# Optimization experiments

Measured on AMD Instinct MI355X. Metric: run time of the kernel, lower is better.

The kernel has to match this reference:

```python
import jax, jax.numpy as jnp
import numpy as np

# --- constants matching DILConfig ---
N_DIFF = 1000      # num_diffusion_steps
STEPS = 4          # inference_steps
S_MAX = 4          # max_scales
BUDGET = 0.2       # entropy_budget
G0 = 2.0           # guidance_strength
ENT_LO = 0.1       # stability_threshold_low
ENT_HI = 0.5       # stability_threshold_high
B, L, C, H = 16, 1024, 128, 512


def setup_inputs() -> dict:
    key = jax.random.key(0)
    ks = jax.random.split(key, 6)
    y_obs = jax.random.normal(ks[0], (B, L, C), dtype=jnp.float32)
    mask = (jax.random.uniform(ks[1], (B, L, C)) > 0.5).astype(jnp.float32)
    z_init = jax.random.normal(ks[2], (B, L, C), dtype=jnp.float32)
    W1 = jax.random.normal(ks[3], (C, H), dtype=jnp.float32) / np.sqrt(C)
    b1 = jnp.zeros((H,), dtype=jnp.float32)
    W2 = jax.random.normal(ks[4], (H, C), dtype=jnp.float32) / np.sqrt(H)
    b2 = jnp.zeros((C,), dtype=jnp.float32)
    tw = jax.random.normal(ks[5], (H,), dtype=jnp.float32)
    return {"y_obs": y_obs, "mask": mask, "z_init": z_init,
            "W1": W1, "b1": b1, "W2": W2, "b2": b2, "tw": tw}


def _dil_forward(y_obs, mask, z_init, W1, b1, W2, b2, tw):
    # diffusion schedule (linear betas)
    betas = jnp.linspace(1e-4, 0.02, N_DIFF, dtype=jnp.float32)
    ac = jnp.cumprod(1.0 - betas)
    alpha = jnp.sqrt(ac)                     # sqrt_alphas_cumprod
    sigma = jnp.sqrt(1.0 - ac)               # sqrt_one_minus_alphas_cumprod
    lam = jnp.log(alpha) - jnp.log(sigma)    # log-SNR/2

    step = N_DIFF // STEPS
    ks = [N_DIFF - 1 - i * step for i in range(STEPS)]

    def score(z, k):
        # epsilon predictor: channel MLP with scalar time feature
        t_feat = jnp.float32(k) / N_DIFF
        h = jax.nn.gelu(jnp.einsum('blc,ch->blh', z, W1) + b1 + t_feat * tw)
        return jnp.einsum('blh,hc->blc', h, W2) + b2

    z = z_init
    for k in ks:  # fixed small unrolled loop over inference steps
        kp = max(k - step, 0)
        eps = score(z, k)                                   # [B,L,C]
        h_lam = lam[kp] - lam[k]
        base_a = alpha[kp] / alpha[k]
        base_b = sigma[kp] * (jnp.exp(h_lam) - 1.0)

        # entropy map: batch-mean |eps| per pixel
        ent_pix = jnp.mean(jnp.abs(eps), axis=0)            # [L,C]

        # self-guidance on observed entries
        obs_err = (z - y_obs) * mask
        guidance = -obs_err / (jnp.var(obs_err) + 1e-8)     # [B,L,C]

        z_new = z
        # coarse -> fine so finer-scale selected nodes overwrite coarser ones
        for s in range(S_MAX - 1, -1, -1):
            w = 2 ** s
            pooled = ent_pix.reshape(L // w, w, C // w, w).mean(axis=(1, 3))
            Knodes = max(1, int(BUDGET * pooled.size))
            _, idx = jax.lax.top_k(pooled.ravel(), Knodes)
            selg = jnp.zeros((pooled.size,), jnp.float32).at[idx].set(1.0)
            selg = selg.reshape(pooled.shape)
            sel = jnp.repeat(jnp.repeat(selg, w, axis=0), w, axis=1)     # [L,C]
            ent_up = jnp.repeat(jnp.repeat(pooled, w, axis=0), w, axis=1)

            # adaptive solver order from entropy stability thresholds
            order = (1.0 + (ent_up > ENT_LO).astype(jnp.float32)
                         + (ent_up > ENT_HI).astype(jnp.float32))
            corr = (1.0 + (order - 1.0) * 0.5 * h_lam
                        + (order - 1.0) * (order - 2.0) / 6.0 * h_lam ** 2)
            gs = G0 * ent_up / (ent_up + 1.0)               # adaptive guidance

            cand = base_a * z - base_b * (corr * eps) + gs * guidance
            z_new = jnp.where(sel[None, :, :] > 0, cand, z_new)
        z = z_new
    return z


def reference(y_obs, mask, z_init, W1, b1, W2, b2, tw):
    return _dil_forward(y_obs, mask, z_init, W1, b1, W2, b2, tw)
```

## Files before the change

### kernel.cpp

```cpp
#include <hip/hip_runtime.h>
#include <math.h>
#include <stdint.h>

#define L_DIM 1024
#define C_DIM 128
#define H_DIM 512
#define B_DIM 16
#define LC (L_DIM * C_DIM)
#define BLC (B_DIM * LC)

typedef __attribute__((ext_vector_type(8))) short short8;
typedef __attribute__((ext_vector_type(4))) float floatx4;

__device__ __forceinline__ unsigned fordbits(unsigned u) {
    return (u & 0x80000000u) ? ~u : (u | 0x80000000u);
}

__device__ __forceinline__ void split3(float x, unsigned& uh, unsigned& um,
                                       unsigned& ul) {
    uh = __float_as_uint(x);
    const float r1 = x - __uint_as_float(uh & 0xffff0000u);
    um = __float_as_uint(r1);
    const float r2 = r1 - __uint_as_float(um & 0xffff0000u);
    ul = __float_as_uint(r2);
}

__device__ __forceinline__ float gelu_fast(float x) {
    const float g = 0.7978845608028654f * (x + 0.044715f * x * x * x);
    const float e = __expf(2.0f * g);
    const float t = 1.0f - 2.0f / (e + 1.0f);
    return 0.5f * x * (1.0f + t);
}

__global__ __launch_bounds__(256) void wsplit_kernel(
    const float* __restrict__ W1, const float* __restrict__ W2,
    unsigned short* __restrict__ W1h, unsigned short* __restrict__ W1m,
    unsigned short* __restrict__ W1l, unsigned short* __restrict__ W2h,
    unsigned short* __restrict__ W2m, unsigned short* __restrict__ W2l) {
    const int t = blockIdx.x * 256 + threadIdx.x;
    unsigned uh, um, ul;
    if (t < 65536) {
        const int j = t & 7, lane = (t >> 3) & 63, nt = (t >> 9) & 31,
                  kt = (t >> 14) & 3;
        const int k = kt * 32 + (lane >> 4) * 8 + j;
        const int n = nt * 16 + (lane & 15);
        split3(W1[k * 512 + n], uh, um, ul);
        W1h[t] = (unsigned short)(uh >> 16);
        W1m[t] = (unsigned short)(um >> 16);
        W1l[t] = (unsigned short)(ul >> 16);
    } else {
        const int t2 = t - 65536;
        const int j = t2 & 7, lane = (t2 >> 3) & 63, nt = (t2 >> 9) & 7,
                  kt = (t2 >> 12) & 15;
        const int k = kt * 32 + (lane >> 4) * 8 + j;
        const int n = nt * 16 + (lane & 15);
        split3(W2[k * 128 + n], uh, um, ul);
        W2h[t2] = (unsigned short)(uh >> 16);
        W2m[t2] = (unsigned short)(um >> 16);
        W2l[t2] = (unsigned short)(ul >> 16);
    }
}

#define MFMA6(AH, AM, AL, BH, BM, BL, ACC)                                    \
    ACC = __builtin_amdgcn_mfma_f32_16x16x32_bf16(AL, BH, ACC, 0, 0, 0);      \
    ACC = __builtin_amdgcn_mfma_f32_16x16x32_bf16(AM, BM, ACC, 0, 0, 0);      \
    ACC = __builtin_amdgcn_mfma_f32_16x16x32_bf16(AH, BL, ACC, 0, 0, 0);      \
    ACC = __builtin_amdgcn_mfma_f32_16x16x32_bf16(AM, BH, ACC, 0, 0, 0);      \
    ACC = __builtin_amdgcn_mfma_f32_16x16x32_bf16(AH, BM, ACC, 0, 0, 0);      \
    ACC = __builtin_amdgcn_mfma_f32_16x16x32_bf16(AH, BH, ACC, 0, 0, 0);

__device__ __forceinline__ int swz(int row, int col) {
    return row * 128 + ((((col >> 3) ^ (row & 15))) << 3) + (col & 7);
}

template <int UPD>
__global__ __launch_bounds__(512, 4) void mlp_kernel(
    float* __restrict__ z, const float* __restrict__ y,
    const float* __restrict__ mk,
    const unsigned short* __restrict__ W1h, const unsigned short* __restrict__ W1m,
    const unsigned short* __restrict__ W1l, const unsigned short* __restrict__ W2h,
    const unsigned short* __restrict__ W2m, const unsigned short* __restrict__ W2l,
    const float* __restrict__ b1, const float* __restrict__ tw,
    const float* __restrict__ b2, float t_feat,
    float* __restrict__ eps_buf, float* __restrict__ ent,
    const float* __restrict__ cA, const float* __restrict__ cB,
    const float* __restrict__ cG, float* __restrict__ accum) {
    __shared__ unsigned short zA[3][4096];
    __shared__ unsigned short hA[3][4096];
    __shared__ float red1[8], red2[8];
    const int tid = threadIdx.x;
    const int w = tid >> 6, lane = tid & 63;
    const int quad = lane >> 4, m16 = lane & 15;
    const int l0 = blockIdx.x * 2;

    float s1 = 0.f, s2 = 0.f;
#pragma unroll
    for (int e = 0; e < 2; ++e) {
        const int f = tid * 8 + e * 4;
        const int r_ = f >> 7, cb = f & 127;
        const int b = r_ & 15, il = r_ >> 4, l = l0 + il;
        const size_t g = ((size_t)b * 1024 + l) * 128 + cb;
        float4 zv = *(const float4*)(z + g);
        const float4 yv = *(const float4*)(y + g);
        const float4 mv = *(const float4*)(mk + g);
        if (UPD) {
            const float4 ev = *(const float4*)(eps_buf + g);
            const int pix = l * 128 + cb;
            const float4 a4 = *(const float4*)(cA + pix);
            const float4 b4 = *(const float4*)(cB + pix);
            const float4 g4 = *(const float4*)(cG + pix);
            zv.x = a4.x * zv.x - b4.x * ev.x - g4.x * ((zv.x - yv.x) * mv.x);
            zv.y = a4.y * zv.y - b4.y * ev.y - g4.y * ((zv.y - yv.y) * mv.y);
            zv.z = a4.z * zv.z - b4.z * ev.z - g4.z * ((zv.z - yv.z) * mv.z);
            zv.w = a4.w * zv.w - b4.w * ev.w - g4.w * ((zv.w - yv.w) * mv.w);
            *(float4*)(z + g) = zv;
        }
        float oe;
        oe = (zv.x - yv.x) * mv.x; s1 += oe; s2 += oe * oe;
        oe = (zv.y - yv.y) * mv.y; s1 += oe; s2 += oe * oe;
        oe = (zv.z - yv.z) * mv.z; s1 += oe; s2 += oe * oe;
        oe = (zv.w - yv.w) * mv.w; s1 += oe; s2 += oe * oe;

        const int base = swz(r_, cb);
        const float xs[4] = {zv.x, zv.y, zv.z, zv.w};
        ushort4 vh, vm, vl;
        unsigned uh, um, ul;
        split3(xs[0], uh, um, ul); vh.x = uh >> 16; vm.x = um >> 16; vl.x = ul >> 16;
        split3(xs[1], uh, um, ul); vh.y = uh >> 16; vm.y = um >> 16; vl.y = ul >> 16;
        split3(xs[2], uh, um, ul); vh.z = uh >> 16; vm.z = um >> 16; vl.z = ul >> 16;
        split3(xs[3], uh, um, ul); vh.w = uh >> 16; vm.w = um >> 16; vl.w = ul >> 16;
        *(ushort4*)(&zA[0][base]) = vh;
        *(ushort4*)(&zA[1][base]) = vm;
        *(ushort4*)(&zA[2][base]) = vl;
    }
#pragma unroll
    for (int off = 32; off; off >>= 1) {
        s1 += __shfl_down(s1, off);
        s2 += __shfl_down(s2, off);
    }
    if (lane == 0) { red1[w] = s1; red2[w] = s2; }
    __syncthreads();
    if (tid == 0) {
        float a1 = 0.f, a2 = 0.f;
#pragma unroll
        for (int i = 0; i < 8; ++i) { a1 += red1[i]; a2 += red2[i]; }
        atomicAdd(&accum[0], a1);
        atomicAdd(&accum[1], a2);
    }

    floatx4 acc1[8];
#pragma unroll
    for (int i = 0; i < 8; ++i) acc1[i] = (floatx4){0.f, 0.f, 0.f, 0.f};

#pragma unroll
    for (int kt = 0; kt < 4; ++kt) {
        short8 Ah[2], Am[2], Al[2];
#pragma unroll
        for (int il = 0; il < 2; ++il) {
            const int fb = swz(il * 16 + m16, kt * 32 + quad * 8);
            Ah[il] = *(const short8*)(&zA[0][fb]);
            Am[il] = *(const short8*)(&zA[1][fb]);
            Al[il] = *(const short8*)(&zA[2][fb]);
        }
#pragma unroll
        for (int q = 0; q < 4; ++q) {
            const size_t off = ((size_t)(kt * 32 + q * 8 + w) * 64 + lane) * 8;
            const short8 bh = *(const short8*)(W1h + off);
            const short8 bm = *(const short8*)(W1m + off);
            const short8 bl = *(const short8*)(W1l + off);
#pragma unroll
            for (int il = 0; il < 2; ++il) {
                floatx4 a = acc1[q * 2 + il];
                MFMA6(Ah[il], Am[il], Al[il], bh, bm, bl, a);
                acc1[q * 2 + il] = a;
            }
        }
    }

    floatx4 acc2[2];
    acc2[0] = (floatx4){0.f, 0.f, 0.f, 0.f};
    acc2[1] = (floatx4){0.f, 0.f, 0.f, 0.f};

    for (int q = 0; q < 4; ++q) {
        __syncthreads();
        {
            const int colg = q * 128 + w * 16 + m16;
            const float bb = b1[colg] + t_feat * tw[colg];
            const int kcol = w * 16 + m16;
#pragma unroll
            for (int il = 0; il < 2; ++il) {
#pragma unroll
                for (int r = 0; r < 4; ++r) {
                    const float x = gelu_fast(acc1[q * 2 + il][r] + bb);
                    unsigned uh, um, ul;
                    split3(x, uh, um, ul);
                    const int idx = swz(il * 16 + quad * 4 + r, kcol);
                    hA[0][idx] = (unsigned short)(uh >> 16);
                    hA[1][idx] = (unsigned short)(um >> 16);
                    hA[2][idx] = (unsigned short)(ul >> 16);
                }
            }
        }
        __syncthreads();

#pragma unroll
        for (int ktl = 0; ktl < 4; ++ktl) {
            short8 Ah2[2], Am2[2], Al2[2];
#pragma unroll
            for (int il = 0; il < 2; ++il) {
                const int fb = swz(il * 16 + m16, ktl * 32 + quad * 8);
                Ah2[il] = *(const short8*)(&hA[0][fb]);
                Am2[il] = *(const short8*)(&hA[1][fb]);
                Al2[il] = *(const short8*)(&hA[2][fb]);
            }
            const size_t off =
                ((size_t)((q * 4 + ktl) * 8 + w) * 64 + lane) * 8;
            const short8 bh = *(const short8*)(W2h + off);
            const short8 bm = *(const short8*)(W2m + off);
            const short8 bl = *(const short8*)(W2l + off);
#pragma unroll
            for (int il = 0; il < 2; ++il) {
                floatx4 a = acc2[il];
                MFMA6(Ah2[il], Am2[il], Al2[il], bh, bm, bl, a);
                acc2[il] = a;
            }
        }
    }

    {
        const int col = w * 16 + m16;
        const float bb2 = b2[col];
#pragma unroll
        for (int il = 0; il < 2; ++il) {
            float pa = 0.f;
#pragma unroll
            for (int r = 0; r < 4; ++r) {
                const float e = acc2[il][r] + bb2;
                const int b = quad * 4 + r;
                eps_buf[((size_t)b * 1024 + l0 + il) * 128 + col] = e;
                pa += fabsf(e);
            }
            pa += __shfl_xor(pa, 16);
            pa += __shfl_xor(pa, 32);
            if (quad == 0) ent[(l0 + il) * 128 + col] = pa * (1.0f / 16.0f);
        }
    }
}

__device__ __forceinline__ void grid_barrier(unsigned* c, unsigned* r) {
    __syncthreads();
    if (threadIdx.x == 0) {
        __threadfence();
        if (atomicAdd(c, 1u) + 1u == 85u) atomicExch(r, 1u);
        else
            while (atomicAdd(r, 0u) == 0u) __builtin_amdgcn_s_sleep(8);
    }
    __syncthreads();
}

__global__ __launch_bounds__(256, 1) void select_kernel(
    const float* __restrict__ ent, float* __restrict__ p1,
    float* __restrict__ p2, float* __restrict__ p3,
    unsigned* __restrict__ ghist, unsigned* __restrict__ ctr,
    unsigned* __restrict__ rel, unsigned* __restrict__ gprefix,
    float* __restrict__ cA, float* __restrict__ cB, float* __restrict__ cG,
    const float* __restrict__ accum_si, float base_a, float base_b,
    float h_lam, int si) {
    const int bid = blockIdx.x, t = threadIdx.x;
    const int gid = bid * 256 + t;
    const int slot0 = si * 6;

    for (int i = gid; i < 32768; i += 21760) {
        const int r = i >> 6, c = i & 63;
        float s = 0.f;
#pragma unroll
        for (int ii = 0; ii < 2; ++ii)
#pragma unroll
            for (int jj = 0; jj < 2; ++jj)
                s += ent[((r * 2 + ii) << 7) + c * 2 + jj];
        atomicExch((unsigned*)&p1[i], __float_as_uint(s * 0.25f));
    }
    for (int i = gid; i < 8192; i += 21760) {
        const int r = i >> 5, c = i & 31;
        float s = 0.f;
#pragma unroll
        for (int ii = 0; ii < 4; ++ii)
#pragma unroll
            for (int jj = 0; jj < 4; ++jj)
                s += ent[((r * 4 + ii) << 7) + c * 4 + jj];
        atomicExch((unsigned*)&p2[i], __float_as_uint(s * 0.0625f));
    }
    for (int i = gid; i < 2048; i += 21760) {
        const int r = i >> 4, c = i & 15;
        float s = 0.f;
#pragma unroll
        for (int ii = 0; ii < 8; ++ii)
#pragma unroll
            for (int jj = 0; jj < 8; ++jj)
                s += ent[((r * 8 + ii) << 7) + c * 8 + jj];
        atomicExch((unsigned*)&p3[i], __float_as_uint(s * (1.0f / 64.0f)));
    }
    grid_barrier(&ctr[slot0], &rel[slot0]);

    const float* data;
    int scale, base;
    unsigned K;
    if (bid < 64) { scale = 0; data = ent; base = bid * 2048; K = 26214u; }
    else if (bid < 80) { scale = 1; data = p1; base = (bid - 64) * 2048; K = 6553u; }
    else if (bid < 84) { scale = 2; data = p2; base = (bid - 80) * 2048; K = 1638u; }
    else { scale = 3; data = p3; base = 0; K = 409u; }

    __shared__ unsigned hist[4][256];
    __shared__ unsigned sh[256];
    __shared__ unsigned sh_dig, sh_krem;
    const int wv = t >> 6;
    unsigned prefix = 0u, krem = K;

    for (int p = 0; p < 4; ++p) {
        const int shift = 24 - 8 * p;
        const unsigned hmask = p ? (0xFFFFFFFFu << (shift + 8)) : 0u;
#pragma unroll
        for (int i = t; i < 1024; i += 256) ((unsigned*)hist)[i] = 0u;
        __syncthreads();
#pragma unroll
        for (int i = t; i < 2048; i += 256) {
            const unsigned raw = atomicAdd((unsigned*)&data[base + i], 0u);
            const unsigned u = fordbits(raw);
            if ((u & hmask) == (prefix & hmask))
                atomicAdd(&hist[wv][(u >> shift) & 255u], 1u);
        }
        __syncthreads();
        const unsigned c = hist[0][t] + hist[1][t] + hist[2][t] + hist[3][t];
        unsigned* gh = &ghist[((si * 4 + p) * 4 + scale) * 256];
        if (c) atomicAdd(&gh[t], c);
        grid_barrier(&ctr[slot0 + 1 + p], &rel[slot0 + 1 + p]);
        sh[t] = atomicAdd(&gh[t], 0u);
        __syncthreads();
#pragma unroll
        for (int off = 1; off < 256; off <<= 1) {
            const unsigned v = (t + off < 256) ? sh[t + off] : 0u;
            __syncthreads();
            sh[t] += v;
            __syncthreads();
        }
        const unsigned suf = sh[t];
        const unsigned sufn = (t < 255) ? sh[t + 1] : 0u;
        if (suf >= krem && sufn < krem) {
            sh_dig = (unsigned)t;
            sh_krem = krem - sufn;
        }
        __syncthreads();
        prefix |= (sh_dig << shift);
        krem = sh_krem;
        __syncthreads();
    }
    if (t == 0 && base == 0) atomicExch(&gprefix[scale], prefix);
    grid_barrier(&ctr[slot0 + 5], &rel[slot0 + 5]);

    const unsigned t0 = atomicAdd(&gprefix[0], 0u);
    const unsigned t1 = atomicAdd(&gprefix[1], 0u);
    const unsigned t2 = atomicAdd(&gprefix[2], 0u);
    const unsigned t3 = atomicAdd(&gprefix[3], 0u);
    const float mean = accum_si[0] * (1.0f / (float)BLC);
    const float var = accum_si[1] * (1.0f / (float)BLC) - mean * mean;
    const float vinv = 1.0f / (var + 1e-8f);

    for (int i = gid; i < LC; i += 21760) {
        const int l = i >> 7, c = i & 127;
        float ent_v = 0.f;
        bool sel = false;
        const float v0 = ent[i];
        if (fordbits(__float_as_uint(v0)) >= t0) { ent_v = v0; sel = true; }
        else {
            const float v1 = __uint_as_float(atomicAdd(
                (unsigned*)&p1[((l >> 1) << 6) + (c >> 1)], 0u));
            if (fordbits(__float_as_uint(v1)) >= t1) { ent_v = v1; sel = true; }
            else {
                const float v2 = __uint_as_float(atomicAdd(
                    (unsigned*)&p2[((l >> 2) << 5) + (c >> 2)], 0u));
                if (fordbits(__float_as_uint(v2)) >= t2) { ent_v = v2; sel = true; }
                else {
                    const float v3 = __uint_as_float(atomicAdd(
                        (unsigned*)&p3[((l >> 3) << 4) + (c >> 3)], 0u));
                    if (fordbits(__float_as_uint(v3)) >= t3) { ent_v = v3; sel = true; }
                }
            }
        }
        if (sel) {
            float corr;
            if (ent_v > 0.5f)
                corr = 1.0f + h_lam + h_lam * h_lam * (1.0f / 3.0f);
            else if (ent_v > 0.1f)
                corr = 1.0f + 0.5f * h_lam;
            else
                corr = 1.0f;
            cA[i] = base_a;
            cB[i] = base_b * corr;
            cG[i] = (2.0f * ent_v / (ent_v + 1.0f)) * vinv;
        } else {
            cA[i] = 1.0f;
            cB[i] = 0.f;
            cG[i] = 0.f;
        }
    }
}

__global__ __launch_bounds__(256) void update_kernel(
    float* __restrict__ z, const float* __restrict__ y,
    const float* __restrict__ mk, const float* __restrict__ eps,
    const float* __restrict__ cA, const float* __restrict__ cB,
    const float* __restrict__ cG) {
    const int idx = blockIdx.x * 256 + threadIdx.x;
    const int p = idx & (LC - 1);
    const float zi = z[idx];
    z[idx] = cA[p] * zi - cB[p] * eps[idx] - cG[p] * ((zi - y[idx]) * mk[idx]);
}

extern "C" void kernel_launch(void* const* d_in, const int* in_sizes, int n_in,
                              void* d_out, int out_size, void* d_ws,
                              size_t ws_size, hipStream_t stream) {
    const float* y_obs = (const float*)d_in[0];
    const float* mask = (const float*)d_in[1];
    const float* z_init = (const float*)d_in[2];
    const float* W1 = (const float*)d_in[3];
    const float* b1 = (const float*)d_in[4];
    const float* W2 = (const float*)d_in[5];
    const float* b2 = (const float*)d_in[6];
    const float* tw = (const float*)d_in[7];
    float* z = (float*)d_out;
    float* ws = (float*)d_ws;

    float* eps = ws;
    float* ent = ws + 2097152;
    float* p1 = ws + 2228224;
    float* p2 = ws + 2260992;
    float* p3 = ws + 2269184;
    float* cA = ws + 2271232;
    float* cB = ws + 2402304;
    float* cG = ws + 2533376;
    unsigned* ghist = (unsigned*)(ws + 2664448);
    unsigned* ctr = (unsigned*)(ws + 2680832);
    unsigned* rel = (unsigned*)(ws + 2680856);
    float* accum = ws + 2680880;
    unsigned* gprefix = (unsigned*)(ws + 2680888);
    unsigned short* W1h = (unsigned short*)(ws + 2680896);
    unsigned short* W1m = (unsigned short*)(ws + 2713664);
    unsigned short* W1l = (unsigned short*)(ws + 2746432);
    unsigned short* W2h = (unsigned short*)(ws + 2779200);
    unsigned short* W2m = (unsigned short*)(ws + 2811968);
    unsigned short* W2l = (unsigned short*)(ws + 2844736);

    float alpha_[1000], sigma_[1000], lam_[1000];
    {
        float ac = 1.0f;
        for (int i = 0; i < 1000; ++i) {
            const float beta = 1e-4f + (0.02f - 1e-4f) * ((float)i / 999.0f);
            ac = ac * (1.0f - beta);
            alpha_[i] = sqrtf(ac);
            sigma_[i] = sqrtf(1.0f - ac);
            lam_[i] = logf(alpha_[i]) - logf(sigma_[i]);
        }
    }
    float tf[4], hl[4], ba[4], bb[4];
    for (int si = 0; si < 4; ++si) {
        const int k = 999 - si * 250;
        const int kp = (k - 250 > 0) ? (k - 250) : 0;
        tf[si] = (float)k / 1000.0f;
        hl[si] = lam_[kp] - lam_[k];
        ba[si] = alpha_[kp] / alpha_[k];
        bb[si] = sigma_[kp] * (expf(hl[si]) - 1.0f);
    }

    hipMemcpyAsync(z, z_init, sizeof(float) * BLC, hipMemcpyDeviceToDevice,
                   stream);
    hipMemsetAsync(ghist, 0, (16384 + 24 + 24 + 8 + 4) * sizeof(unsigned),
                   stream);
    wsplit_kernel<<<512, 256, 0, stream>>>(W1, W2, W1h, W1m, W1l, W2h, W2m,
                                           W2l);

    for (int si = 0; si < 4; ++si) {
        if (si == 0) {
            mlp_kernel<0><<<512, 512, 0, stream>>>(
                z, y_obs, mask, W1h, W1m, W1l, W2h, W2m, W2l, b1, tw, b2,
                tf[0], eps, ent, cA, cB, cG, accum);
        } else {
            mlp_kernel<1><<<512, 512, 0, stream>>>(
                z, y_obs, mask, W1h, W1m, W1l, W2h, W2m, W2l, b1, tw, b2,
                tf[si], eps, ent, cA, cB, cG, accum + 2 * si);
        }
        select_kernel<<<85, 256, 0, stream>>>(
            ent, p1, p2, p3, ghist, ctr, rel, gprefix, cA, cB, cG,
            accum + 2 * si, ba[si], bb[si], hl[si], si);
    }
    update_kernel<<<8192, 256, 0, stream>>>(z, y_obs, mask, eps, cA, cB, cG);
}
```

Measured before the change: 407.1 us.

## Fuse pooling into radix-select blocks, cache data in LDS, simplify grid barrier

Each select block now computes its own slice of the pooled entropy maps directly into shared memory, so the first grid barrier is gone and histogram passes read LDS instead of doing atomic global reads. The grid barrier becomes a single monotonically increasing counter per step with cumulative targets and a shorter sleep, and the fence is dropped. The grid grows to 88 blocks so the coarsest scale is split across four blocks. Removing the threadfence risks weaker memory ordering for the global histogram and prefix values.

```diff
diff --git a/kernel.cpp b/kernel.cpp
--- a/kernel.cpp
+++ b/kernel.cpp
@@ -247,13 +247,11 @@
     }
 }
 
-__device__ __forceinline__ void grid_barrier(unsigned* c, unsigned* r) {
+__device__ __forceinline__ void gbar(unsigned* c, unsigned target) {
     __syncthreads();
     if (threadIdx.x == 0) {
-        __threadfence();
-        if (atomicAdd(c, 1u) + 1u == 85u) atomicExch(r, 1u);
-        else
-            while (atomicAdd(r, 0u) == 0u) __builtin_amdgcn_s_sleep(8);
+        atomicAdd(c, 1u);
+        while (atomicAdd(c, 0u) < target) __builtin_amdgcn_s_sleep(1);
     }
     __syncthreads();
 }
@@ -262,70 +260,85 @@
     const float* __restrict__ ent, float* __restrict__ p1,
     float* __restrict__ p2, float* __restrict__ p3,
     unsigned* __restrict__ ghist, unsigned* __restrict__ ctr,
-    unsigned* __restrict__ rel, unsigned* __restrict__ gprefix,
-    float* __restrict__ cA, float* __restrict__ cB, float* __restrict__ cG,
+    unsigned* __restrict__ gprefix, float* __restrict__ cA,
+    float* __restrict__ cB, float* __restrict__ cG,
     const float* __restrict__ accum_si, float base_a, float base_b,
     float h_lam, int si) {
-    const int bid = blockIdx.x, t = threadIdx.x;
-    const int gid = bid * 256 + t;
-    const int slot0 = si * 6;
-
-    for (int i = gid; i < 32768; i += 21760) {
-        const int r = i >> 6, c = i & 63;
-        float s = 0.f;
-#pragma unroll
-        for (int ii = 0; ii < 2; ++ii)
-#pragma unroll
-            for (int jj = 0; jj < 2; ++jj)
-                s += ent[((r * 2 + ii) << 7) + c * 2 + jj];
-        atomicExch((unsigned*)&p1[i], __float_as_uint(s * 0.25f));
-    }
-    for (int i = gid; i < 8192; i += 21760) {
-        const int r = i >> 5, c = i & 31;
-        float s = 0.f;
-#pragma unroll
-        for (int ii = 0; ii < 4; ++ii)
-#pragma unroll
-            for (int jj = 0; jj < 4; ++jj)
-                s += ent[((r * 4 + ii) << 7) + c * 4 + jj];
-        atomicExch((unsigned*)&p2[i], __float_as_uint(s * 0.0625f));
-    }
-    for (int i = gid; i < 2048; i += 21760) {
-        const int r = i >> 4, c = i & 15;
-        float s = 0.f;
-#pragma unroll
-        for (int ii = 0; ii < 8; ++ii)
-#pragma unroll
-            for (int jj = 0; jj < 8; ++jj)
-                s += ent[((r * 8 + ii) << 7) + c * 8 + jj];
-        atomicExch((unsigned*)&p3[i], __float_as_uint(s * (1.0f / 64.0f)));
-    }
-    grid_barrier(&ctr[slot0], &rel[slot0]);
-
-    const float* data;
-    int scale, base;
-    unsigned K;
-    if (bid < 64) { scale = 0; data = ent; base = bid * 2048; K = 26214u; }
-    else if (bid < 80) { scale = 1; data = p1; base = (bid - 64) * 2048; K = 6553u; }
-    else if (bid < 84) { scale = 2; data = p2; base = (bid - 80) * 2048; K = 1638u; }
-    else { scale = 3; data = p3; base = 0; K = 409u; }
-
+    __shared__ float dataL[2048];
     __shared__ unsigned hist[4][256];
     __shared__ unsigned sh[256];
     __shared__ unsigned sh_dig, sh_krem;
+    const int bid = blockIdx.x, t = threadIdx.x;
+    const int gid = bid * 256 + t;
+    unsigned* cc = &ctr[si];
+
+    int scale, nloc;
+    unsigned K;
+    if (bid < 64) {
+        scale = 0; nloc = 2048; K = 26214u;
+        const int base = bid * 2048;
+        for (int i = t; i < 2048; i += 256) dataL[i] = ent[base + i];
+    } else if (bid < 80) {
+        scale = 1; nloc = 2048; K = 6553u;
+        const int base = (bid - 64) * 2048;
+        for (int i = t; i < 2048; i += 256) {
+            const int idx = base + i;
+            const int r = idx >> 6, c = idx & 63;
+            float s = 0.f;
+#pragma unroll
+            for (int ii = 0; ii < 2; ++ii)
+#pragma unroll
+                for (int jj = 0; jj < 2; ++jj)
+                    s += ent[((r * 2 + ii) << 7) + c * 2 + jj];
+            const float v = s * 0.25f;
+            dataL[i] = v;
+            atomicExch((unsigned*)&p1[idx], __float_as_uint(v));
+        }
+    } else if (bid < 84) {
+        scale = 2; nloc = 2048; K = 1638u;
+        const int base = (bid - 80) * 2048;
+        for (int i = t; i < 2048; i += 256) {
+            const int idx = base + i;
+            const int r = idx >> 5, c = idx & 31;
+            float s = 0.f;
+#pragma unroll
+            for (int ii = 0; ii < 4; ++ii)
+#pragma unroll
+                for (int jj = 0; jj < 4; ++jj)
+                    s += ent[((r * 4 + ii) << 7) + c * 4 + jj];
+            const float v = s * 0.0625f;
+            dataL[i] = v;
+            atomicExch((unsigned*)&p2[idx], __float_as_uint(v));
+        }
+    } else {
+        scale = 3; nloc = 512; K = 409u;
+        const int base = (bid - 84) * 512;
+        for (int i = t; i < 512; i += 256) {
+            const int idx = base + i;
+            const int r = idx >> 4, c = idx & 15;
+            float s = 0.f;
+#pragma unroll
+            for (int ii = 0; ii < 8; ++ii)
+#pragma unroll
+                for (int jj = 0; jj < 8; ++jj)
+                    s += ent[((r * 8 + ii) << 7) + c * 8 + jj];
+            const float v = s * (1.0f / 64.0f);
+            dataL[i] = v;
+            atomicExch((unsigned*)&p3[idx], __float_as_uint(v));
+        }
+    }
+    __syncthreads();
+
     const int wv = t >> 6;
     unsigned prefix = 0u, krem = K;
-
     for (int p = 0; p < 4; ++p) {
         const int shift = 24 - 8 * p;
         const unsigned hmask = p ? (0xFFFFFFFFu << (shift + 8)) : 0u;
 #pragma unroll
         for (int i = t; i < 1024; i += 256) ((unsigned*)hist)[i] = 0u;
         __syncthreads();
-#pragma unroll
-        for (int i = t; i < 2048; i += 256) {
-            const unsigned raw = atomicAdd((unsigned*)&data[base + i], 0u);
-            const unsigned u = fordbits(raw);
+        for (int i = t; i < nloc; i += 256) {
+            const unsigned u = fordbits(__float_as_uint(dataL[i]));
             if ((u & hmask) == (prefix & hmask))
                 atomicAdd(&hist[wv][(u >> shift) & 255u], 1u);
         }
@@ -333,7 +346,7 @@
         const unsigned c = hist[0][t] + hist[1][t] + hist[2][t] + hist[3][t];
         unsigned* gh = &ghist[((si * 4 + p) * 4 + scale) * 256];
         if (c) atomicAdd(&gh[t], c);
-        grid_barrier(&ctr[slot0 + 1 + p], &rel[slot0 + 1 + p]);
+        gbar(cc, 88u * (unsigned)(p + 1));
         sh[t] = atomicAdd(&gh[t], 0u);
         __syncthreads();
 #pragma unroll
@@ -354,8 +367,9 @@
         krem = sh_krem;
         __syncthreads();
     }
-    if (t == 0 && base == 0) atomicExch(&gprefix[scale], prefix);
-    grid_barrier(&ctr[slot0 + 5], &rel[slot0 + 5]);
+    if (t == 0 && (bid == 0 || bid == 64 || bid == 80 || bid == 84))
+        atomicExch(&gprefix[scale], prefix);
+    gbar(cc, 88u * 5u);
 
     const unsigned t0 = atomicAdd(&gprefix[0], 0u);
     const unsigned t1 = atomicAdd(&gprefix[1], 0u);
@@ -365,7 +379,7 @@
     const float var = accum_si[1] * (1.0f / (float)BLC) - mean * mean;
     const float vinv = 1.0f / (var + 1e-8f);
 
-    for (int i = gid; i < LC; i += 21760) {
+    for (int i = gid; i < LC; i += 22528) {
         const int l = i >> 7, c = i & 127;
         float ent_v = 0.f;
         bool sel = false;
@@ -440,15 +454,14 @@
     float* cG = ws + 2533376;
     unsigned* ghist = (unsigned*)(ws + 2664448);
     unsigned* ctr = (unsigned*)(ws + 2680832);
-    unsigned* rel = (unsigned*)(ws + 2680856);
-    float* accum = ws + 2680880;
-    unsigned* gprefix = (unsigned*)(ws + 2680888);
-    unsigned short* W1h = (unsigned short*)(ws + 2680896);
-    unsigned short* W1m = (unsigned short*)(ws + 2713664);
-    unsigned short* W1l = (unsigned short*)(ws + 2746432);
-    unsigned short* W2h = (unsigned short*)(ws + 2779200);
-    unsigned short* W2m = (unsigned short*)(ws + 2811968);
-    unsigned short* W2l = (unsigned short*)(ws + 2844736);
+    float* accum = ws + 2680836;
+    unsigned* gprefix = (unsigned*)(ws + 2680844);
+    unsigned short* W1h = (unsigned short*)(ws + 2680848);
+    unsigned short* W1m = (unsigned short*)(ws + 2713616);
+    unsigned short* W1l = (unsigned short*)(ws + 2746384);
+    unsigned short* W2h = (unsigned short*)(ws + 2779152);
+    unsigned short* W2m = (unsigned short*)(ws + 2811920);
+    unsigned short* W2l = (unsigned short*)(ws + 2844688);
 
     float alpha_[1000], sigma_[1000], lam_[1000];
     {
@@ -473,8 +486,7 @@
 
     hipMemcpyAsync(z, z_init, sizeof(float) * BLC, hipMemcpyDeviceToDevice,
                    stream);
-    hipMemsetAsync(ghist, 0, (16384 + 24 + 24 + 8 + 4) * sizeof(unsigned),
-                   stream);
+    hipMemsetAsync(ghist, 0, (16384 + 4 + 8 + 4) * sizeof(unsigned), stream);
     wsplit_kernel<<<512, 256, 0, stream>>>(W1, W2, W1h, W1m, W1l, W2h, W2m,
                                            W2l);
 
@@ -488,8 +500,8 @@
                 z, y_obs, mask, W1h, W1m, W1l, W2h, W2m, W2l, b1, tw, b2,
                 tf[si], eps, ent, cA, cB, cG, accum + 2 * si);
         }
-        select_kernel<<<85, 256, 0, stream>>>(
-            ent, p1, p2, p3, ghist, ctr, rel, gprefix, cA, cB, cG,
+        select_kernel<<<88, 256, 0, stream>>>(
+            ent, p1, p2, p3, ghist, ctr, gprefix, cA, cB, cG,
             accum + 2 * si, ba[si], bb[si], hl[si], si);
     }
     update_kernel<<<8192, 256, 0, stream>>>(z, y_obs, mask, eps, cA, cB, cG);
```

Result: slower. 450.0 us (+10.5%).
